# Kernel optimization log

Measured on AMD Instinct MI355X. Metric: run time of the kernel, lower is better.

The kernel has to match this reference:

```python
import jax, jax.numpy as jnp
import numpy as np

B, C, H, W = 64, 64, 56, 56
MID = 2 * C  # two output nodes concatenated
EPS = 1e-5


def _conv1x1(x, w):
    # x: [B,C,H,W], w: [O,C] (1x1 conv kernel squeezed)
    return jnp.einsum('bchw,oc->bohw', x, w)


def _bn(x, g, b, m, v):
    # eval-mode BatchNorm2d with running stats
    sc = g * jax.lax.rsqrt(v + EPS)
    return x * sc[None, :, None, None] + (b - m * sc)[None, :, None, None]


def _maxpool3(x):
    # MaxPool2d(kernel=3, stride=1, padding=1)
    return jax.lax.reduce_window(x, -jnp.inf, jax.lax.max,
                                 (1, 1, 3, 3), (1, 1, 1, 1),
                                 [(0, 0), (0, 0), (1, 1), (1, 1)])


def _avgpool3(x):
    # AvgPool2d(kernel=3, stride=1, padding=1), count_include_pad=True -> /9
    s = jax.lax.reduce_window(x, 0.0, jax.lax.add,
                              (1, 1, 3, 3), (1, 1, 1, 1),
                              [(0, 0), (0, 0), (1, 1), (1, 1)])
    return s * (1.0 / 9.0)


def setup_inputs() -> dict:
    key = jax.random.key(0)
    ks = jax.random.split(key, 11)
    x = jax.random.normal(ks[0], (B, C, H, W), dtype=jnp.float32)
    w1 = jax.random.normal(ks[1], (C, C), dtype=jnp.float32) * 0.1
    w2 = jax.random.normal(ks[2], (C, MID), dtype=jnp.float32) * 0.1
    bn1_g = 1.0 + 0.1 * jax.random.normal(ks[3], (C,), dtype=jnp.float32)
    bn1_b = 0.1 * jax.random.normal(ks[4], (C,), dtype=jnp.float32)
    bn1_m = 0.1 * jax.random.normal(ks[5], (C,), dtype=jnp.float32)
    bn1_v = jax.random.uniform(ks[6], (C,), minval=0.5, maxval=1.5, dtype=jnp.float32)
    bn2_g = 1.0 + 0.1 * jax.random.normal(ks[7], (C,), dtype=jnp.float32)
    bn2_b = 0.1 * jax.random.normal(ks[8], (C,), dtype=jnp.float32)
    bn2_m = 0.1 * jax.random.normal(ks[9], (C,), dtype=jnp.float32)
    bn2_v = jax.random.uniform(ks[10], (C,), minval=0.5, maxval=1.5, dtype=jnp.float32)
    return dict(x=x, w1=w1, w2=w2,
                bn1_g=bn1_g, bn1_b=bn1_b, bn1_m=bn1_m, bn1_v=bn1_v,
                bn2_g=bn2_g, bn2_b=bn2_b, bn2_m=bn2_m, bn2_v=bn2_v)


def reference(x, w1, w2, bn1_g, bn1_b, bn1_m, bn1_v, bn2_g, bn2_b, bn2_m, bn2_v):
    # DAG g = [[[0,1],[1,2]], [[4,3],[3]], [[5,3],[3,100]], [[4,3],[100]]]
    # topoSort order: [0, 2, 1, 3]; output nodes (ordered): [2, 3]
    node0 = jax.nn.relu(_bn(_conv1x1(x, w1), bn1_g, bn1_b, bn1_m, bn1_v))
    node1 = _maxpool3(node0)            # op type 4, pred {0}
    node2 = _avgpool3(node0)            # op type 5, pred {0}
    node3 = _maxpool3(node1) + _maxpool3(node2)  # op type 4, preds {1,2}, summed
    cat = jnp.concatenate([node2, node3], axis=1)  # [B, 2C, H, W]
    out = jax.nn.relu(_bn(_conv1x1(cat, w2), bn2_g, bn2_b, bn2_m, bn2_v))
    return out
```

## Files before the change

### kernel.cpp

```cpp
#include <hip/hip_runtime.h>
#include <cstddef>

#define EPS 1e-5f
static constexpr int Bn = 64, Cn = 64, Hn = 56, Wn = 56, HWn = Hn * Wn;
static constexpr int XS = 65;

typedef __attribute__((ext_vector_type(8))) short short8;
typedef __attribute__((ext_vector_type(8))) unsigned short ushort8;
typedef __attribute__((ext_vector_type(4))) float floatx4;
typedef __attribute__((ext_vector_type(16))) float floatx16;
typedef __attribute__((ext_vector_type(4))) unsigned int uintx4;
typedef __attribute__((ext_vector_type(2))) unsigned int uintx2;

__device__ __forceinline__ unsigned pack_rne(float a, float b) {
    unsigned ua = __float_as_uint(a), ub = __float_as_uint(b);
    ua = ua + 0x7fffu + ((ua >> 16) & 1u);
    ub = ub + 0x7fffu + ((ub >> 16) & 1u);
    return __builtin_amdgcn_perm(ub, ua, 0x07060302);
}
__device__ __forceinline__ unsigned pack_trunc(float a, float b) {
    return __builtin_amdgcn_perm(__float_as_uint(b), __float_as_uint(a), 0x07060302);
}
__device__ __forceinline__ ushort8 pmax(ushort8 a, ushort8 b) {
    return __builtin_elementwise_max(a, b);
}
__device__ __forceinline__ float bf_lo(unsigned u) { return __uint_as_float(u << 16); }
__device__ __forceinline__ float bf_hi(unsigned u) { return __uint_as_float(u & 0xffff0000u); }


__global__ __launch_bounds__(256) void k1_conv1(
    const float* __restrict__ x, const float* __restrict__ w1,
    const float* __restrict__ bg, const float* __restrict__ bb,
    const float* __restrict__ bm, const float* __restrict__ bv,
    unsigned short* __restrict__ node0)
{
    __shared__ float xs[2][64 * XS];
    __shared__ float scs[64], shs[64];
    const int tid = threadIdx.x;
    if (tid < 64) {
        float sc = bg[tid] * rsqrtf(bv[tid] + EPS);
        scs[tid] = sc;
        shs[tid] = bb[tid] - bm[tid] * sc;
    }
    __syncthreads();
    const int lane = tid & 63;
    const int wv   = tid >> 6;
    const int m    = lane & 15;
    const int quad = lane >> 4;
    const int qoff = quad * 8;

    short8 afr[4][2];
    float shv[16];
    #pragma unroll
    for (int t = 0; t < 4; ++t) {
        const float sc = scs[t * 16 + m];
        #pragma unroll
        for (int kk = 0; kk < 2; ++kk) {
            const float* wp = w1 + (t * 16 + m) * 64 + kk * 32 + qoff;
            floatx4 f0 = *(const floatx4*)wp;
            floatx4 f1 = *(const floatx4*)(wp + 4);
            uintx4 u;
            u.x = pack_rne(f0[0] * sc, f0[1] * sc);
            u.y = pack_rne(f0[2] * sc, f0[3] * sc);
            u.z = pack_rne(f1[0] * sc, f1[1] * sc);
            u.w = pack_rne(f1[2] * sc, f1[3] * sc);
            afr[t][kk] = *(short8*)&u;
        }
        #pragma unroll
        for (int i = 0; i < 4; ++i) shv[t * 4 + i] = shs[t * 16 + quad * 4 + i];
    }

    floatx4 stg[4];
    auto ldtile = [&](int tt) {
        const int P = blockIdx.x * 256 + tt * 64;
        const int b = P / HWn, p0 = P - b * HWn;
        #pragma unroll
        for (int q = 0; q < 4; ++q) {
            int idx = q * 256 + tid;
            int c = idx >> 4, f = idx & 15;
            stg[q] = *(const floatx4*)(x + (size_t)(b * 64 + c) * HWn + p0 + f * 4);
        }
    };
    auto sttile = [&](int buf) {
        #pragma unroll
        for (int q = 0; q < 4; ++q) {
            int idx = q * 256 + tid;
            int c = idx >> 4, f = idx & 15;
            #pragma unroll
            for (int k = 0; k < 4; ++k)
                xs[buf][(f * 4 + k) * XS + c] = stg[q][k];
        }
    };

    ldtile(0);
    sttile(0);

    #pragma unroll
    for (int tt = 0; tt < 4; ++tt) {
        __syncthreads();
        if (tt < 3) ldtile(tt + 1);

        const int P = blockIdx.x * 256 + tt * 64;
        const int b = P / HWn, p0 = P - b * HWn;
        const float* xr = &xs[tt & 1][(wv * 16 + m) * XS];

        floatx4 acc[4];
        #pragma unroll
        for (int t = 0; t < 4; ++t) acc[t] = (floatx4){0.f, 0.f, 0.f, 0.f};

        #pragma unroll
        for (int kk = 0; kk < 2; ++kk) {
            float f[8];
            #pragma unroll
            for (int j = 0; j < 8; ++j) f[j] = xr[kk * 32 + qoff + j];
            uintx4 u;
            u.x = pack_trunc(f[0], f[1]);
            u.y = pack_trunc(f[2], f[3]);
            u.z = pack_trunc(f[4], f[5]);
            u.w = pack_trunc(f[6], f[7]);
            short8 bfr = *(short8*)&u;
            #pragma unroll
            for (int t = 0; t < 4; ++t)
                acc[t] = __builtin_amdgcn_mfma_f32_16x16x32_bf16(afr[t][kk], bfr, acc[t], 0, 0, 0);
        }

        const int chunkbase = (quad >> 1);
        const int j0 = (quad & 1) * 4;
        #pragma unroll
        for (int t = 0; t < 4; ++t) {
            float v0 = acc[t][0] + shv[t * 4 + 0]; v0 = v0 > 0.f ? v0 : 0.f;
            float v1 = acc[t][1] + shv[t * 4 + 1]; v1 = v1 > 0.f ? v1 : 0.f;
            float v2 = acc[t][2] + shv[t * 4 + 2]; v2 = v2 > 0.f ? v2 : 0.f;
            float v3 = acc[t][3] + shv[t * 4 + 3]; v3 = v3 > 0.f ? v3 : 0.f;
            uintx2 st;
            st.x = pack_rne(v0, v1);
            st.y = pack_rne(v2, v3);
            int chunk = t * 2 + chunkbase;
            *(uintx2*)(node0 + ((size_t)(b * 8 + chunk) * HWn + p0 + wv * 16 + m) * 8 + j0) = st;
        }

        if (tt < 3) sttile((tt + 1) & 1);
    }
}

__global__ __launch_bounds__(256) void k2_pools(
    const unsigned short* __restrict__ node0, unsigned short* __restrict__ cat)
{
    const int tid = threadIdx.x;
    const int lane = tid & 63;
    const int wv = tid >> 6;
    const int bid = blockIdx.x;
    const int half = bid & 1;
    const int band = (bid >> 1) % 7;
    const int b = bid / 14;
    const int chunk = half * 4 + wv;
    const int lo = band * 8;
    const int col = lane;
    const bool act = col < Wn;
    const unsigned short* base = node0 + ((size_t)(b * 8 + chunk) * HWn) * 8;
    unsigned short* cavg = cat + ((size_t)(b * 16 + chunk) * HWn) * 8;
    unsigned short* cmax = cat + ((size_t)(b * 16 + 8 + chunk) * HWn) * 8;

    const ushort8 zz = (ushort8)0;
    auto load5 = [&](int r, ushort8* d) {
        #pragma unroll
        for (int dd = 0; dd < 5; ++dd) {
            int cc = col + dd - 2;
            bool ok = act && ((unsigned)cc < (unsigned)Wn) && ((unsigned)r < (unsigned)Hn);
            d[dd] = ok ? *(const ushort8*)(base + (size_t)(r * Wn + cc) * 8) : zz;
        }
    };

    float hs1[8], hs2[8];
    ushort8 h5a = zz, h5b = zz, h5c = zz, h5d = zz, nh1 = zz, nh2 = zz;
    #pragma unroll
    for (int j = 0; j < 8; ++j) hs1[j] = hs2[j] = 0.f;

    ushort8 d[5];
    load5(lo - 2, d);

    #pragma unroll
    for (int i = 0; i < 12; ++i) {
        const int r = lo - 2 + i;
        ushort8 dn[5];
        if (i < 11) load5(r + 1, dn);

        ushort8 hm5 = pmax(pmax(pmax(d[0], d[1]), pmax(d[2], d[3])), d[4]);
        ushort8 m5 = pmax(pmax(pmax(h5a, h5b), pmax(h5c, h5d)), hm5);
        h5a = h5b; h5b = h5c; h5c = h5d; h5d = hm5;

        const uintx4 ul = *(const uintx4*)&d[1];
        const uintx4 uv = *(const uintx4*)&d[2];
        const uintx4 ur = *(const uintx4*)&d[3];
        float a2[8];
        const int r2 = r - 1, r3 = r - 2;
        const bool v2 = (unsigned)r2 < (unsigned)Hn;
        #pragma unroll
        for (int w = 0; w < 4; ++w) {
            float hsum0 = bf_lo(ul[w]) + bf_lo(uv[w]) + bf_lo(ur[w]);
            float hsum1 = bf_hi(ul[w]) + bf_hi(uv[w]) + bf_hi(ur[w]);
            a2[w * 2 + 0] = v2 ? (hs2[w * 2 + 0] + hs1[w * 2 + 0] + hsum0) * (1.f / 9.f) : 0.f;
            a2[w * 2 + 1] = v2 ? (hs2[w * 2 + 1] + hs1[w * 2 + 1] + hsum1) * (1.f / 9.f) : 0.f;
            hs2[w * 2 + 0] = hs1[w * 2 + 0]; hs1[w * 2 + 0] = hsum0;
            hs2[w * 2 + 1] = hs1[w * 2 + 1]; hs1[w * 2 + 1] = hsum1;
        }
        uintx4 ap;
        ap.x = pack_rne(a2[0], a2[1]);
        ap.y = pack_rne(a2[2], a2[3]);
        ap.z = pack_rne(a2[4], a2[5]);
        ap.w = pack_rne(a2[6], a2[7]);
        uintx4 al, ar;
        #pragma unroll
        for (int w = 0; w < 4; ++w) {
            unsigned u = ap[w];
            unsigned lu = __shfl_up(u, 1);
            unsigned ru = __shfl_down(u, 1);
            al[w] = (lane == 0) ? 0u : lu;
            ar[w] = (lane == 63) ? 0u : ru;
        }
        ushort8 nh = pmax(pmax(*(ushort8*)&al, *(ushort8*)&ap), *(ushort8*)&ar);
        ushort8 m3 = pmax(pmax(nh2, nh1), nh);
        nh2 = nh1; nh1 = nh;

        if (act && r2 >= lo && r2 < lo + 8)
            *(uintx4*)(cavg + (size_t)(r2 * Wn + col) * 8) = ap;
        if (act && r3 >= lo && r3 < lo + 8) {
            const uintx4 u5 = *(const uintx4*)&m5;
            const uintx4 u3 = *(const uintx4*)&m3;
            uintx4 st;
            #pragma unroll
            for (int w = 0; w < 4; ++w)
                st[w] = pack_rne(bf_lo(u5[w]) + bf_lo(u3[w]), bf_hi(u5[w]) + bf_hi(u3[w]));
            *(uintx4*)(cmax + (size_t)(r3 * Wn + col) * 8) = st;
        }
        #pragma unroll
        for (int dd = 0; dd < 5; ++dd) d[dd] = dn[dd];
    }
}

__global__ __launch_bounds__(256) void k3_conv2(
    const unsigned short* __restrict__ cat, const float* __restrict__ w2,
    const float* __restrict__ bg, const float* __restrict__ bb,
    const float* __restrict__ bm, const float* __restrict__ bv,
    float* __restrict__ out)
{
    __shared__ unsigned short wl[1024 * 8];
    __shared__ float scs[64], shs[64];
    const int tid = threadIdx.x;
    if (tid < 64) {
        float sc = bg[tid] * rsqrtf(bv[tid] + EPS);
        scs[tid] = sc;
        shs[tid] = bb[tid] - bm[tid] * sc;
    }
    #pragma unroll
    for (int q = 0; q < 4; ++q) {
        int ci = tid * 4 + q;
        int lane_ = ci & 63, tk = ci >> 6;
        int t = tk >> 3, kt = tk & 7, n_ = lane_ & 31, h_ = lane_ >> 5;
        const float* wp = w2 + (t * 32 + n_) * 128 + kt * 16 + h_ * 8;
        floatx4 f0 = *(const floatx4*)wp;
        floatx4 f1 = *(const floatx4*)(wp + 4);
        uintx4 u;
        u.x = pack_rne(f0[0], f0[1]);
        u.y = pack_rne(f0[2], f0[3]);
        u.z = pack_rne(f1[0], f1[1]);
        u.w = pack_rne(f1[2], f1[3]);
        *(uintx4*)(wl + (size_t)ci * 8) = u;
    }
    __syncthreads();

    const int lane = tid & 63;
    const int wv = tid >> 6;
    const int n = lane & 31;
    const int h = lane >> 5;

    short8 afr[2][8];
    #pragma unroll
    for (int t = 0; t < 2; ++t)
        #pragma unroll
        for (int kt = 0; kt < 8; ++kt)
            afr[t][kt] = *(const short8*)(wl + ((size_t)((t * 8 + kt) * 64 + lane)) * 8);

    #pragma unroll
    for (int s = 0; s < 2; ++s) {
        const int tile = (blockIdx.x * 4 + wv) * 2 + s;
        const int b = tile / 98;
        const int p0 = (tile - b * 98) * 32;

        floatx16 acc0, acc1;
        #pragma unroll
        for (int i = 0; i < 16; ++i) { acc0[i] = 0.f; acc1[i] = 0.f; }

        #pragma unroll
        for (int kt = 0; kt < 8; ++kt) {
            short8 bfr = *(const short8*)(cat + ((size_t)(b * 16 + kt * 2 + h) * HWn + p0 + n) * 8);
            acc0 = __builtin_amdgcn_mfma_f32_32x32x16_bf16(afr[0][kt], bfr, acc0, 0, 0, 0);
            acc1 = __builtin_amdgcn_mfma_f32_32x32x16_bf16(afr[1][kt], bfr, acc1, 0, 0, 0);
        }

        float* ob = out + (size_t)b * 64 * HWn + p0 + n;
        #pragma unroll
        for (int r = 0; r < 16; ++r) {
            int o = (r & 3) + 8 * (r >> 2) + 4 * h;
            float v0 = fmaf(acc0[r], scs[o], shs[o]);
            ob[(size_t)o * HWn] = v0 > 0.f ? v0 : 0.f;
            float v1 = fmaf(acc1[r], scs[o + 32], shs[o + 32]);
            ob[(size_t)(o + 32) * HWn] = v1 > 0.f ? v1 : 0.f;
        }
    }
}

extern "C" void kernel_launch(void* const* d_in, const int* in_sizes, int n_in,
                              void* d_out, int out_size, void* d_ws, size_t ws_size,
                              hipStream_t stream)
{
    const float* x   = (const float*)d_in[0];
    const float* w1  = (const float*)d_in[1];
    const float* w2  = (const float*)d_in[2];
    const float* b1g = (const float*)d_in[3];
    const float* b1b = (const float*)d_in[4];
    const float* b1m = (const float*)d_in[5];
    const float* b1v = (const float*)d_in[6];
    const float* b2g = (const float*)d_in[7];
    const float* b2b = (const float*)d_in[8];
    const float* b2m = (const float*)d_in[9];
    const float* b2v = (const float*)d_in[10];

    float* out = (float*)d_out;
    unsigned short* node0 = (unsigned short*)d_ws;
    unsigned short* cat   = node0 + (size_t)Bn * HWn * 64;

    k1_conv1<<<dim3(784), dim3(256), 0, stream>>>(x, w1, b1g, b1b, b1m, b1v, node0);
    k2_pools<<<dim3(Bn * 14), dim3(256), 0, stream>>>(node0, cat);
    k3_conv2<<<dim3(784), dim3(256), 0, stream>>>(cat, w2, b2g, b2b, b2m, b2v, out);
}
```

Measured before the change: 161.3 us.

## Fuse pooling and second 1x1 conv into one kernel via LDS-resident cat tile

Merges the pooling kernel and the second conv kernel into a single kernel. Each 512-thread block computes the avg-pool and max-pool branches for one batch and an 8-row band across all channels, and writes them into shared memory instead of a global cat buffer. It then runs 16x16x32 bf16 MFMAs straight from that LDS tile and applies BN+ReLU on output. This removes the global write and reread of the cat tensor and one launch. The cost is about 115KB of LDS per block, which limits occupancy, and it also swizzles the block order.

```diff
diff --git a/kernel.cpp b/kernel.cpp
--- a/kernel.cpp
+++ b/kernel.cpp
@@ -4,6 +4,10 @@
 #define EPS 1e-5f
 static constexpr int Bn = 64, Cn = 64, Hn = 56, Wn = 56, HWn = Hn * Wn;
 static constexpr int XS = 65;
+static constexpr int RB = 8;
+static constexpr int NBAND = 7;
+static constexpr int BPX = RB * Wn;
+static constexpr int SLAB = 3600;
 
 typedef __attribute__((ext_vector_type(8))) short short8;
 typedef __attribute__((ext_vector_type(8))) unsigned short ushort8;
@@ -143,121 +147,34 @@
     }
 }
 
-__global__ __launch_bounds__(256) void k2_pools(
-    const unsigned short* __restrict__ node0, unsigned short* __restrict__ cat)
-{
-    const int tid = threadIdx.x;
-    const int lane = tid & 63;
-    const int wv = tid >> 6;
-    const int bid = blockIdx.x;
-    const int half = bid & 1;
-    const int band = (bid >> 1) % 7;
-    const int b = bid / 14;
-    const int chunk = half * 4 + wv;
-    const int lo = band * 8;
-    const int col = lane;
-    const bool act = col < Wn;
-    const unsigned short* base = node0 + ((size_t)(b * 8 + chunk) * HWn) * 8;
-    unsigned short* cavg = cat + ((size_t)(b * 16 + chunk) * HWn) * 8;
-    unsigned short* cmax = cat + ((size_t)(b * 16 + 8 + chunk) * HWn) * 8;
-
-    const ushort8 zz = (ushort8)0;
-    auto load5 = [&](int r, ushort8* d) {
-        #pragma unroll
-        for (int dd = 0; dd < 5; ++dd) {
-            int cc = col + dd - 2;
-            bool ok = act && ((unsigned)cc < (unsigned)Wn) && ((unsigned)r < (unsigned)Hn);
-            d[dd] = ok ? *(const ushort8*)(base + (size_t)(r * Wn + cc) * 8) : zz;
-        }
-    };
-
-    float hs1[8], hs2[8];
-    ushort8 h5a = zz, h5b = zz, h5c = zz, h5d = zz, nh1 = zz, nh2 = zz;
-    #pragma unroll
-    for (int j = 0; j < 8; ++j) hs1[j] = hs2[j] = 0.f;
-
-    ushort8 d[5];
-    load5(lo - 2, d);
-
-    #pragma unroll
-    for (int i = 0; i < 12; ++i) {
-        const int r = lo - 2 + i;
-        ushort8 dn[5];
-        if (i < 11) load5(r + 1, dn);
-
-        ushort8 hm5 = pmax(pmax(pmax(d[0], d[1]), pmax(d[2], d[3])), d[4]);
-        ushort8 m5 = pmax(pmax(pmax(h5a, h5b), pmax(h5c, h5d)), hm5);
-        h5a = h5b; h5b = h5c; h5c = h5d; h5d = hm5;
-
-        const uintx4 ul = *(const uintx4*)&d[1];
-        const uintx4 uv = *(const uintx4*)&d[2];
-        const uintx4 ur = *(const uintx4*)&d[3];
-        float a2[8];
-        const int r2 = r - 1, r3 = r - 2;
-        const bool v2 = (unsigned)r2 < (unsigned)Hn;
-        #pragma unroll
-        for (int w = 0; w < 4; ++w) {
-            float hsum0 = bf_lo(ul[w]) + bf_lo(uv[w]) + bf_lo(ur[w]);
-            float hsum1 = bf_hi(ul[w]) + bf_hi(uv[w]) + bf_hi(ur[w]);
-            a2[w * 2 + 0] = v2 ? (hs2[w * 2 + 0] + hs1[w * 2 + 0] + hsum0) * (1.f / 9.f) : 0.f;
-            a2[w * 2 + 1] = v2 ? (hs2[w * 2 + 1] + hs1[w * 2 + 1] + hsum1) * (1.f / 9.f) : 0.f;
-            hs2[w * 2 + 0] = hs1[w * 2 + 0]; hs1[w * 2 + 0] = hsum0;
-            hs2[w * 2 + 1] = hs1[w * 2 + 1]; hs1[w * 2 + 1] = hsum1;
-        }
-        uintx4 ap;
-        ap.x = pack_rne(a2[0], a2[1]);
-        ap.y = pack_rne(a2[2], a2[3]);
-        ap.z = pack_rne(a2[4], a2[5]);
-        ap.w = pack_rne(a2[6], a2[7]);
-        uintx4 al, ar;
-        #pragma unroll
-        for (int w = 0; w < 4; ++w) {
-            unsigned u = ap[w];
-            unsigned lu = __shfl_up(u, 1);
-            unsigned ru = __shfl_down(u, 1);
-            al[w] = (lane == 0) ? 0u : lu;
-            ar[w] = (lane == 63) ? 0u : ru;
-        }
-        ushort8 nh = pmax(pmax(*(ushort8*)&al, *(ushort8*)&ap), *(ushort8*)&ar);
-        ushort8 m3 = pmax(pmax(nh2, nh1), nh);
-        nh2 = nh1; nh1 = nh;
-
-        if (act && r2 >= lo && r2 < lo + 8)
-            *(uintx4*)(cavg + (size_t)(r2 * Wn + col) * 8) = ap;
-        if (act && r3 >= lo && r3 < lo + 8) {
-            const uintx4 u5 = *(const uintx4*)&m5;
-            const uintx4 u3 = *(const uintx4*)&m3;
-            uintx4 st;
-            #pragma unroll
-            for (int w = 0; w < 4; ++w)
-                st[w] = pack_rne(bf_lo(u5[w]) + bf_lo(u3[w]), bf_hi(u5[w]) + bf_hi(u3[w]));
-            *(uintx4*)(cmax + (size_t)(r3 * Wn + col) * 8) = st;
-        }
-        #pragma unroll
-        for (int dd = 0; dd < 5; ++dd) d[dd] = dn[dd];
-    }
-}
-
-__global__ __launch_bounds__(256) void k3_conv2(
-    const unsigned short* __restrict__ cat, const float* __restrict__ w2,
+__global__ __launch_bounds__(512) void k23_fused(
+    const unsigned short* __restrict__ node0,
+    const float* __restrict__ w2,
     const float* __restrict__ bg, const float* __restrict__ bb,
     const float* __restrict__ bm, const float* __restrict__ bv,
     float* __restrict__ out)
 {
-    __shared__ unsigned short wl[1024 * 8];
-    __shared__ float scs[64], shs[64];
+    __shared__ __align__(16) unsigned short catl[16 * SLAB];
     const int tid = threadIdx.x;
-    if (tid < 64) {
-        float sc = bg[tid] * rsqrtf(bv[tid] + EPS);
-        scs[tid] = sc;
-        shs[tid] = bb[tid] - bm[tid] * sc;
-    }
-    #pragma unroll
-    for (int q = 0; q < 4; ++q) {
-        int ci = tid * 4 + q;
-        int lane_ = ci & 63, tk = ci >> 6;
-        int t = tk >> 3, kt = tk & 7, n_ = lane_ & 31, h_ = lane_ >> 5;
-        const float* wp = w2 + (t * 32 + n_) * 128 + kt * 16 + h_ * 8;
+    const int lane = tid & 63;
+    const int wv = tid >> 6;
+
+    int bid = blockIdx.x;
+    bid = (bid & 7) * 56 + (bid >> 3);
+    const int band = bid % NBAND;
+    const int b = bid / NBAND;
+    const int lo = band * RB;
+
+    const int m = lane & 15;
+    const int q = lane >> 4;
+    const int t = wv >> 1;
+
+    short8 afr[4];
+    #pragma unroll
+    for (int cp = 0; cp < 4; ++cp) {
+        const int c = 2 * cp + (q >> 1);
+        const int chb = ((q & 1) ? 64 : 0) + 8 * c;
+        const float* wp = w2 + (size_t)(t * 16 + m) * 128 + chb;
         floatx4 f0 = *(const floatx4*)wp;
         floatx4 f1 = *(const floatx4*)(wp + 4);
         uintx4 u;
@@ -265,47 +182,128 @@
         u.y = pack_rne(f0[2], f0[3]);
         u.z = pack_rne(f1[0], f1[1]);
         u.w = pack_rne(f1[2], f1[3]);
-        *(uintx4*)(wl + (size_t)ci * 8) = u;
+        afr[cp] = *(short8*)&u;
+    }
+    const int oc0 = t * 16 + q * 4;
+    floatx4 g4 = *(const floatx4*)(bg + oc0);
+    floatx4 bb4 = *(const floatx4*)(bb + oc0);
+    floatx4 mm4 = *(const floatx4*)(bm + oc0);
+    floatx4 vv4 = *(const floatx4*)(bv + oc0);
+    float sc[4], sh[4];
+    #pragma unroll
+    for (int r = 0; r < 4; ++r) {
+        sc[r] = g4[r] * rsqrtf(vv4[r] + EPS);
+        sh[r] = bb4[r] - mm4[r] * sc[r];
+    }
+
+    {
+        const int chunk = wv;
+        const int col = lane;
+        const bool act = col < Wn;
+        const unsigned short* base = node0 + ((size_t)(b * 8 + chunk) * HWn) * 8;
+        unsigned short* cav = catl + (size_t)(chunk * 2 + 0) * SLAB;
+        unsigned short* cmx = catl + (size_t)(chunk * 2 + 1) * SLAB;
+
+        const ushort8 zz = (ushort8)0;
+        auto load5 = [&](int r, ushort8* d) {
+            #pragma unroll
+            for (int dd = 0; dd < 5; ++dd) {
+                int cc = col + dd - 2;
+                bool ok = act && ((unsigned)cc < (unsigned)Wn) && ((unsigned)r < (unsigned)Hn);
+                d[dd] = ok ? *(const ushort8*)(base + (size_t)(r * Wn + cc) * 8) : zz;
+            }
+        };
+
+        float hs1[8], hs2[8];
+        ushort8 h5a = zz, h5b = zz, h5c = zz, h5d = zz, nh1 = zz, nh2 = zz;
+        #pragma unroll
+        for (int j = 0; j < 8; ++j) hs1[j] = hs2[j] = 0.f;
+
+        ushort8 d[5];
+        load5(lo - 2, d);
+
+        #pragma unroll
+        for (int i = 0; i < 12; ++i) {
+            const int r = lo - 2 + i;
+            ushort8 dn[5];
+            if (i < 11) load5(r + 1, dn);
+
+            ushort8 hm5 = pmax(pmax(pmax(d[0], d[1]), pmax(d[2], d[3])), d[4]);
+            ushort8 m5 = pmax(pmax(pmax(h5a, h5b), pmax(h5c, h5d)), hm5);
+            h5a = h5b; h5b = h5c; h5c = h5d; h5d = hm5;
+
+            const uintx4 ul = *(const uintx4*)&d[1];
+            const uintx4 uv = *(const uintx4*)&d[2];
+            const uintx4 ur = *(const uintx4*)&d[3];
+            float a2[8];
+            const int r2 = r - 1, r3 = r - 2;
+            const bool v2 = (unsigned)r2 < (unsigned)Hn;
+            #pragma unroll
+            for (int w = 0; w < 4; ++w) {
+                float hsum0 = bf_lo(ul[w]) + bf_lo(uv[w]) + bf_lo(ur[w]);
+                float hsum1 = bf_hi(ul[w]) + bf_hi(uv[w]) + bf_hi(ur[w]);
+                a2[w * 2 + 0] = v2 ? (hs2[w * 2 + 0] + hs1[w * 2 + 0] + hsum0) * (1.f / 9.f) : 0.f;
+                a2[w * 2 + 1] = v2 ? (hs2[w * 2 + 1] + hs1[w * 2 + 1] + hsum1) * (1.f / 9.f) : 0.f;
+                hs2[w * 2 + 0] = hs1[w * 2 + 0]; hs1[w * 2 + 0] = hsum0;
+                hs2[w * 2 + 1] = hs1[w * 2 + 1]; hs1[w * 2 + 1] = hsum1;
+            }
+            uintx4 ap;
+            ap.x = pack_rne(a2[0], a2[1]);
+            ap.y = pack_rne(a2[2], a2[3]);
+            ap.z = pack_rne(a2[4], a2[5]);
+            ap.w = pack_rne(a2[6], a2[7]);
+            uintx4 al, ar;
+            #pragma unroll
+            for (int w = 0; w < 4; ++w) {
+                unsigned u = ap[w];
+                unsigned lu = __shfl_up(u, 1);
+                unsigned ru = __shfl_down(u, 1);
+                al[w] = (lane == 0) ? 0u : lu;
+                ar[w] = (lane == 63) ? 0u : ru;
+            }
+            ushort8 nh = pmax(pmax(*(ushort8*)&al, *(ushort8*)&ap), *(ushort8*)&ar);
+            ushort8 m3 = pmax(pmax(nh2, nh1), nh);
+            nh2 = nh1; nh1 = nh;
+
+            if (act && r2 >= lo && r2 < lo + RB)
+                *(uintx4*)(cav + (size_t)((r2 - lo) * Wn + col) * 8) = ap;
+            if (act && r3 >= lo && r3 < lo + RB) {
+                const uintx4 u5 = *(const uintx4*)&m5;
+                const uintx4 u3 = *(const uintx4*)&m3;
+                uintx4 st;
+                #pragma unroll
+                for (int w = 0; w < 4; ++w)
+                    st[w] = pack_rne(bf_lo(u5[w]) + bf_lo(u3[w]), bf_hi(u5[w]) + bf_hi(u3[w]));
+                *(uintx4*)(cmx + (size_t)((r3 - lo) * Wn + col) * 8) = st;
+            }
+            #pragma unroll
+            for (int dd = 0; dd < 5; ++dd) d[dd] = dn[dd];
+        }
     }
     __syncthreads();
 
-    const int lane = tid & 63;
-    const int wv = tid >> 6;
-    const int n = lane & 31;
-    const int h = lane >> 5;
-
-    short8 afr[2][8];
-    #pragma unroll
-    for (int t = 0; t < 2; ++t)
-        #pragma unroll
-        for (int kt = 0; kt < 8; ++kt)
-            afr[t][kt] = *(const short8*)(wl + ((size_t)((t * 8 + kt) * 64 + lane)) * 8);
-
-    #pragma unroll
-    for (int s = 0; s < 2; ++s) {
-        const int tile = (blockIdx.x * 4 + wv) * 2 + s;
-        const int b = tile / 98;
-        const int p0 = (tile - b * 98) * 32;
-
-        floatx16 acc0, acc1;
-        #pragma unroll
-        for (int i = 0; i < 16; ++i) { acc0[i] = 0.f; acc1[i] = 0.f; }
-
-        #pragma unroll
-        for (int kt = 0; kt < 8; ++kt) {
-            short8 bfr = *(const short8*)(cat + ((size_t)(b * 16 + kt * 2 + h) * HWn + p0 + n) * 8);
-            acc0 = __builtin_amdgcn_mfma_f32_32x32x16_bf16(afr[0][kt], bfr, acc0, 0, 0, 0);
-            acc1 = __builtin_amdgcn_mfma_f32_32x32x16_bf16(afr[1][kt], bfr, acc1, 0, 0, 0);
-        }
-
-        float* ob = out + (size_t)b * 64 * HWn + p0 + n;
-        #pragma unroll
-        for (int r = 0; r < 16; ++r) {
-            int o = (r & 3) + 8 * (r >> 2) + 4 * h;
-            float v0 = fmaf(acc0[r], scs[o], shs[o]);
-            ob[(size_t)o * HWn] = v0 > 0.f ? v0 : 0.f;
-            float v1 = fmaf(acc1[r], scs[o + 32], shs[o + 32]);
-            ob[(size_t)(o + 32) * HWn] = v1 > 0.f ? v1 : 0.f;
+    floatx4 acc[14];
+    #pragma unroll
+    for (int i = 0; i < 14; ++i) acc[i] = (floatx4){0.f, 0.f, 0.f, 0.f};
+
+    #pragma unroll
+    for (int cp = 0; cp < 4; ++cp) {
+        #pragma unroll
+        for (int i = 0; i < 14; ++i) {
+            const int px = ((wv & 1) * 14 + i) * 16 + m;
+            short8 bfr = *(const short8*)(catl + (size_t)(4 * cp + q) * SLAB + (size_t)px * 8);
+            acc[i] = __builtin_amdgcn_mfma_f32_16x16x32_bf16(afr[cp], bfr, acc[i], 0, 0, 0);
+        }
+    }
+
+    float* ob = out + (size_t)(b * 64 + oc0) * HWn + lo * Wn;
+    #pragma unroll
+    for (int i = 0; i < 14; ++i) {
+        const int px = ((wv & 1) * 14 + i) * 16 + m;
+        #pragma unroll
+        for (int r = 0; r < 4; ++r) {
+            float v = fmaf(acc[i][r], sc[r], sh[r]);
+            ob[(size_t)r * HWn + px] = v > 0.f ? v : 0.f;
         }
     }
 }
@@ -328,9 +326,7 @@
 
     float* out = (float*)d_out;
     unsigned short* node0 = (unsigned short*)d_ws;
-    unsigned short* cat   = node0 + (size_t)Bn * HWn * 64;
 
     k1_conv1<<<dim3(784), dim3(256), 0, stream>>>(x, w1, b1g, b1b, b1m, b1v, node0);
-    k2_pools<<<dim3(Bn * 14), dim3(256), 0, stream>>>(node0, cat);
-    k3_conv2<<<dim3(784), dim3(256), 0, stream>>>(cat, w2, b2g, b2b, b2m, b2v, out);
-}
+    k23_fused<<<dim3(Bn * NBAND), dim3(512), 0, stream>>>(node0, w2, b2g, b2b, b2m, b2v, out);
+}
```

New measurement: 153.0 us. -5.1%, faster.
